# Performance work log

Hardware: AMD Instinct MI355X
Metric: run time of the kernel (lower is better)

The kernel has to match this reference:

```python
import jax, jax.numpy as jnp
import numpy as np

B, T, C = 4, 2048, 2048
N_HEAD = 16
N_KV_HEAD = 4
N_REP = N_HEAD // N_KV_HEAD  # 4
HD = C // N_HEAD             # 128
FC_MULT = 1.0
EPS = 1e-12


def l2norm(x):
    return x / (jnp.linalg.norm(x, axis=-1, keepdims=True) + EPS)


def setup_inputs() -> dict:
    key = jax.random.key(0)
    k1, k2, k3, k4 = jax.random.split(key, 4)
    s = 1.0 / np.sqrt(C)
    return {
        "x": jax.random.normal(k1, (B, T, C), dtype=jnp.float32),
        "Wq": jax.random.normal(k2, (C, C), dtype=jnp.float32) * s,
        "Wkv": jax.random.normal(k3, (C, 2 * C // N_REP), dtype=jnp.float32) * s,
        "Wproj": jax.random.normal(k4, (C, C), dtype=jnp.float32) * s,
    }


def reference(x, Wq, Wkv, Wproj):
    kv_dim = C // N_REP  # 512
    q = FC_MULT * (x @ Wq)                     # [B,T,C]
    kv = FC_MULT * (x @ Wkv)                   # [B,T,2*kv_dim]
    k, v = kv[..., :kv_dim], kv[..., kv_dim:]
    # L2 prenorm over full projection dims (before head split), as in module
    q = l2norm(q)
    k = l2norm(k)
    # split heads; GQA without materializing repeated K/V
    q = q.reshape(B, T, N_KV_HEAD, N_REP, HD)  # [B,T,G,R,H]
    k = k.reshape(B, T, N_KV_HEAD, HD)         # [B,S,G,H]
    v = v.reshape(B, T, N_KV_HEAD, HD)
    scale = 1.0 / np.sqrt(HD)
    scores = jnp.einsum('btgrh,bsgh->bgrts', q, k) * scale  # [B,G,R,T,S]
    causal = jnp.tril(jnp.ones((T, T), dtype=bool))
    scores = jnp.where(causal, scores, -jnp.inf)
    att = jax.nn.softmax(scores, axis=-1)
    y = jnp.einsum('bgrts,bsgh->btgrh', att, v)  # [B,T,G,R,H]
    y = y.reshape(B, T, C)
    return FC_MULT * (y @ Wproj)
```

## Files before the change

kernel.cpp:

```cpp
#include <hip/hip_runtime.h>
#include <hip/hip_bf16.h>
#include <math.h>

#define B_   4
#define T_   2048
#define C_   2048
#define NH_  16
#define HD_  128
#define KVD_ 1024

typedef __attribute__((ext_vector_type(4))) float f32x4;
typedef __attribute__((ext_vector_type(16))) float f32x16;
typedef __attribute__((ext_vector_type(8))) short bf16x8;
typedef __attribute__((ext_vector_type(4))) unsigned int u32x4;

__device__ __forceinline__ void async_copy16(const __hip_bfloat16* g, __hip_bfloat16* l) {
  __builtin_amdgcn_global_load_lds((const __attribute__((address_space(1))) void*)g,
                                   (__attribute__((address_space(3))) void*)l,
                                   16, 0, 0);
}

__device__ __forceinline__ float bf2f(__hip_bfloat16 h) { return __bfloat162float(h); }

__device__ __forceinline__ unsigned int pkbf(float a, float b) {
  float2 f2; f2.x = a; f2.y = b;
  __hip_bfloat162 h2 = __float22bfloat162_rn(f2);
  return *reinterpret_cast<unsigned int*>(&h2);
}

__global__ __launch_bounds__(256) void f32_to_bf16_k(const float* __restrict__ src,
                                                     __hip_bfloat16* __restrict__ dst, int n4) {
  int i = blockIdx.x * 256 + threadIdx.x;
  if (i >= n4) return;
  float4 f = ((const float4*)src)[i];
  __hip_bfloat16 o[4] = {__float2bfloat16(f.x), __float2bfloat16(f.y),
                         __float2bfloat16(f.z), __float2bfloat16(f.w)};
  *(uint2*)(dst + (size_t)i * 4) = *(uint2*)o;
}

__global__ __launch_bounds__(256) void transpose_f32_bf16_k(const float* __restrict__ W,
                                                            __hip_bfloat16* __restrict__ WT,
                                                            int K, int N) {
  __shared__ float tile[32][33];
  int bx = blockIdx.x * 32;
  int by = blockIdx.y * 32;
  int tx = threadIdx.x, ty = threadIdx.y;
  for (int i = ty; i < 32; i += 8)
    tile[i][tx] = W[(size_t)(by + i) * N + (bx + tx)];
  __syncthreads();
  for (int i = ty; i < 32; i += 8)
    WT[(size_t)(bx + i) * K + (by + tx)] = __float2bfloat16(tile[tx][i]);
}

__global__ __launch_bounds__(256) void vtrans_k(const __hip_bfloat16* __restrict__ kv,
                                                __hip_bfloat16* __restrict__ vt) {
  __shared__ __hip_bfloat16 tile[32][33];
  int bg = blockIdx.z;
  int d0 = blockIdx.y * 32;
  int t0 = blockIdx.x * 32;
  int tx = threadIdx.x, ty = threadIdx.y;
  int b = bg >> 2, g = bg & 3;
  const __hip_bfloat16* src = kv + (size_t)b * T_ * KVD_ + 512 + g * HD_;
  for (int i = ty; i < 32; i += 8)
    tile[i][tx] = src[(size_t)(t0 + i) * KVD_ + d0 + tx];
  __syncthreads();
  __hip_bfloat16* dst = vt + (size_t)bg * HD_ * T_;
  int txp = (tx & ~12) | ((tx & 4) << 1) | ((tx & 8) >> 1);
  for (int i = ty; i < 32; i += 8)
    dst[(size_t)(d0 + i) * T_ + t0 + txp] = tile[tx][i];
}

template<int PER>
__global__ __launch_bounds__(256) void rownorm_k(__hip_bfloat16* __restrict__ buf,
                                                 int stride, float extra) {
  const int tid = threadIdx.x;
  __hip_bfloat16* p = buf + (size_t)blockIdx.x * stride;
  float v[PER];
  float ss = 0.f;
  #pragma unroll
  for (int e = 0; e < PER; ++e) { v[e] = bf2f(p[tid + e * 256]); ss += v[e] * v[e]; }
  #pragma unroll
  for (int off = 32; off >= 1; off >>= 1) ss += __shfl_xor(ss, off, 64);
  __shared__ float wsum[4];
  if ((tid & 63) == 0) wsum[tid >> 6] = ss;
  __syncthreads();
  float tot = wsum[0] + wsum[1] + wsum[2] + wsum[3];
  float sc = extra / (sqrtf(tot) + 1e-12f);
  #pragma unroll
  for (int e = 0; e < PER; ++e) p[tid + e * 256] = __float2bfloat16(v[e] * sc);
}

template<typename OutT>
__global__ __launch_bounds__(512, 2) void gemm3_k(const __hip_bfloat16* __restrict__ A,
                                                  const __hip_bfloat16* __restrict__ BT,
                                                  OutT* __restrict__ Cc,
                                                  int M, int N, int K) {
  __shared__ alignas(16) __hip_bfloat16 As[3][128 * 64];
  __shared__ alignas(16) __hip_bfloat16 Bs[3][256 * 64];
  const int tid  = threadIdx.x;
  const int bm   = blockIdx.y * 128;
  const int bn   = blockIdx.x * 256;
  const int wave = tid >> 6, lane = tid & 63;
  const int wm = wave >> 2, wn = wave & 3;
  const int lm = lane & 15, quad = lane >> 4;
  const size_t Kz = (size_t)K;
  const int NT = K >> 6;

  const int srow = tid >> 3;
  const int csw  = ((tid & 7) ^ (srow & 7)) * 8;
  const __hip_bfloat16* aSrc0 = A  + (size_t)(bm + srow) * Kz + csw;
  const __hip_bfloat16* aSrc1 = A  + (size_t)(bm + 64 + srow) * Kz + csw;
  const __hip_bfloat16* bSrc0 = BT + (size_t)(bn + srow) * Kz + csw;
  const __hip_bfloat16* bSrc1 = BT + (size_t)(bn + 64 + srow) * Kz + csw;
  const __hip_bfloat16* bSrc2 = BT + (size_t)(bn + 128 + srow) * Kz + csw;
  const __hip_bfloat16* bSrc3 = BT + (size_t)(bn + 192 + srow) * Kz + csw;

  auto stageA = [&](int slot, int koff) {
    async_copy16(aSrc0 + koff, As[slot] + tid * 8);
    async_copy16(aSrc1 + koff, As[slot] + (512 + tid) * 8);
  };
  auto stageB0 = [&](int slot, int koff) {
    async_copy16(bSrc0 + koff, Bs[slot] + tid * 8);
  };
  auto stageB123 = [&](int slot, int koff) {
    async_copy16(bSrc1 + koff, Bs[slot] + (512 + tid) * 8);
    async_copy16(bSrc2 + koff, Bs[slot] + (1024 + tid) * 8);
    async_copy16(bSrc3 + koff, Bs[slot] + (1536 + tid) * 8);
  };

  const int ch0 = ((quad) ^ (lm & 7)) * 8;
  const int ch1 = ((4 + quad) ^ (lm & 7)) * 8;
  const int arow = wm * 64 + lm;
  const int brow = wn * 64 + lm;

  f32x4 acc[4][4] = {};

  stageA(0, 0); stageB0(0, 0); stageB123(0, 0);
  if (NT > 1) { stageA(1, 64); stageB0(1, 64); stageB123(1, 64); }

  int s = 0;
  for (int t = 0; t < NT; ++t) {
    const int sn = (s + 2 > 2) ? (s - 1) : (s + 2);
    const bool pre = (t + 2) < NT;
    const int koff = (t + 2) * 64;
    if (t + 1 < NT) asm volatile("s_waitcnt vmcnt(6)" ::: "memory");
    else            asm volatile("s_waitcnt vmcnt(0)" ::: "memory");
    __builtin_amdgcn_s_barrier();
    bf16x8 af[4][2], bf0[2][2];
    #pragma unroll
    for (int mf = 0; mf < 4; ++mf) {
      af[mf][0] = *(const bf16x8*)(As[s] + (arow + mf * 16) * 64 + ch0);
      af[mf][1] = *(const bf16x8*)(As[s] + (arow + mf * 16) * 64 + ch1);
    }
    #pragma unroll
    for (int nf = 0; nf < 2; ++nf) {
      bf0[nf][0] = *(const bf16x8*)(Bs[s] + (brow + nf * 16) * 64 + ch0);
      bf0[nf][1] = *(const bf16x8*)(Bs[s] + (brow + nf * 16) * 64 + ch1);
    }
    if (pre) { stageA(sn, koff); stageB0(sn, koff); }
    __builtin_amdgcn_s_barrier();
    __builtin_amdgcn_s_setprio(1);
    #pragma unroll
    for (int mf = 0; mf < 4; ++mf)
      #pragma unroll
      for (int nf = 0; nf < 2; ++nf) {
        acc[mf][nf] = __builtin_amdgcn_mfma_f32_16x16x32_bf16(af[mf][0], bf0[nf][0], acc[mf][nf], 0, 0, 0);
        acc[mf][nf] = __builtin_amdgcn_mfma_f32_16x16x32_bf16(af[mf][1], bf0[nf][1], acc[mf][nf], 0, 0, 0);
      }
    __builtin_amdgcn_s_setprio(0);
    __builtin_amdgcn_s_barrier();
    bf16x8 bf1[2][2];
    #pragma unroll
    for (int nf = 0; nf < 2; ++nf) {
      bf1[nf][0] = *(const bf16x8*)(Bs[s] + (brow + (nf + 2) * 16) * 64 + ch0);
      bf1[nf][1] = *(const bf16x8*)(Bs[s] + (brow + (nf + 2) * 16) * 64 + ch1);
    }
    if (pre) stageB123(sn, koff);
    __builtin_amdgcn_s_barrier();
    __builtin_amdgcn_s_setprio(1);
    #pragma unroll
    for (int mf = 0; mf < 4; ++mf)
      #pragma unroll
      for (int nf = 0; nf < 2; ++nf) {
        acc[mf][nf + 2] = __builtin_amdgcn_mfma_f32_16x16x32_bf16(af[mf][0], bf1[nf][0], acc[mf][nf + 2], 0, 0, 0);
        acc[mf][nf + 2] = __builtin_amdgcn_mfma_f32_16x16x32_bf16(af[mf][1], bf1[nf][1], acc[mf][nf + 2], 0, 0, 0);
      }
    __builtin_amdgcn_s_setprio(0);
    s = (s == 2) ? 0 : s + 1;
  }

  const int r0 = quad * 4;
  #pragma unroll
  for (int mf = 0; mf < 4; ++mf)
    #pragma unroll
    for (int nf = 0; nf < 4; ++nf)
      #pragma unroll
      for (int r = 0; r < 4; ++r) {
        int gr = bm + wm * 64 + mf * 16 + r0 + r;
        int gc = bn + wn * 64 + nf * 16 + lm;
        float v = acc[mf][nf][r];
        if constexpr (__is_same(OutT, float))
          Cc[(size_t)gr * N + gc] = v;
        else
          Cc[(size_t)gr * N + gc] = __float2bfloat16(v);
      }
}

__global__ __launch_bounds__(256, 2) void attn_k(const __hip_bfloat16* __restrict__ q,
                                                 const __hip_bfloat16* __restrict__ kv,
                                                 const __hip_bfloat16* __restrict__ vt,
                                                 __hip_bfloat16* __restrict__ y) {
  const int pp = blockIdx.x;
  const int h  = blockIdx.y;
  const int b  = blockIdx.z;
  const int g  = h >> 2;
  const int tid = threadIdx.x;
  const int wave = tid >> 6, lane = tid & 63;
  const int l31 = lane & 31, hi = lane >> 5;

  __shared__ alignas(16) __hip_bfloat16 Ks[2][64 * 128];
  __shared__ alignas(16) __hip_bfloat16 Vts[2][128 * 64];

  const __hip_bfloat16* kb = kv + (size_t)b * T_ * KVD_ + g * HD_;
  const __hip_bfloat16* vb = vt + (size_t)(b * 4 + g) * HD_ * T_;

  auto stage = [&](int buf, int jt) {
    const size_t j1 = (size_t)jt * 64;
    #pragma unroll
    for (int e = 0; e < 4; ++e) {
      int idx = tid + e * 256;
      int row = idx >> 4, c = idx & 15;
      async_copy16(kb + (j1 + row) * KVD_ + ((c ^ (row & 15)) * 8), Ks[buf] + idx * 8);
    }
    #pragma unroll
    for (int e = 0; e < 4; ++e) {
      int idx = tid + e * 256;
      int row = idx >> 3, c = idx & 7;
      async_copy16(vb + (size_t)row * T_ + j1 + ((c ^ (row & 7)) * 8), Vts[buf] + idx * 8);
    }
  };

  stage(0, 0);

  #pragma unroll
  for (int seg = 0; seg < 2; ++seg) {
    const int qt = seg ? pp : (15 - pp);
    const int qbase = qt * 128 + wave * 32;
    const int qmax = qbase + 31;
    const int ntiles = 2 * qt + 2;

    const __hip_bfloat16* qrow = q + ((size_t)b * T_ + qbase + l31) * C_ + h * HD_;
    bf16x8 qf[8];
    #pragma unroll
    for (int kc = 0; kc < 8; ++kc)
      qf[kc] = *(const bf16x8*)(qrow + kc * 16 + hi * 8);

    __syncthreads();

    f32x16 o_acc[4] = {};
    float l_acc = 0.f;

    for (int it = 0; it < ntiles; ++it) {
      const int cur = it & 1;
      if (it + 1 < ntiles) stage(cur ^ 1, it + 1);
      const int j0 = it * 64;
      if (j0 <= qmax) {
        f32x16 st0 = {}, st1 = {};
        __builtin_amdgcn_s_setprio(1);
        #pragma unroll
        for (int kc = 0; kc < 8; ++kc) {
          const int cs0 = (((2 * kc + hi) ^ (l31 & 15)) * 8);
          bf16x8 k0 = *(const bf16x8*)(Ks[cur] + l31 * 128 + cs0);
          bf16x8 k1 = *(const bf16x8*)(Ks[cur] + (32 + l31) * 128 + cs0);
          st0 = __builtin_amdgcn_mfma_f32_32x32x16_bf16(k0, qf[kc], st0, 0, 0, 0);
          st1 = __builtin_amdgcn_mfma_f32_32x32x16_bf16(k1, qf[kc], st1, 0, 0, 0);
        }
        __builtin_amdgcn_s_setprio(0);
        const int qd = qbase + l31 - j0;
        if (j0 + 63 <= qbase) {
          #pragma unroll
          for (int r = 0; r < 16; ++r) {
            float p0 = __expf(st0[r]);
            float p1 = __expf(st1[r]);
            st0[r] = p0; st1[r] = p1;
            l_acc += p0 + p1;
          }
        } else {
          #pragma unroll
          for (int r = 0; r < 16; ++r) {
            const int ofs = (r & 3) + 8 * (r >> 2) + 4 * hi;
            float p0 = (ofs <= qd) ? __expf(st0[r]) : 0.f;
            float p1 = (ofs + 32 <= qd) ? __expf(st1[r]) : 0.f;
            st0[r] = p0; st1[r] = p1;
            l_acc += p0 + p1;
          }
        }
        unsigned int W[8][2];
        #pragma unroll
        for (int q4 = 0; q4 < 4; ++q4) {
          W[q4][0]     = pkbf(st0[4 * q4 + 0], st0[4 * q4 + 1]);
          W[q4][1]     = pkbf(st0[4 * q4 + 2], st0[4 * q4 + 3]);
          W[4 + q4][0] = pkbf(st1[4 * q4 + 0], st1[4 * q4 + 1]);
          W[4 + q4][1] = pkbf(st1[4 * q4 + 2], st1[4 * q4 + 3]);
        }
        __builtin_amdgcn_s_setprio(1);
        #pragma unroll
        for (int kc = 0; kc < 4; ++kc) {
          u32x4 pw;
          pw[0] = W[2 * kc][0]; pw[1] = W[2 * kc][1];
          pw[2] = W[2 * kc + 1][0]; pw[3] = W[2 * kc + 1][1];
          bf16x8 pf = __builtin_bit_cast(bf16x8, pw);
          const int csv = (((2 * kc + hi) ^ (l31 & 7)) * 8);
          #pragma unroll
          for (int ct = 0; ct < 4; ++ct) {
            bf16x8 vf = *(const bf16x8*)(Vts[cur] + (ct * 32 + l31) * 64 + csv);
            o_acc[ct] = __builtin_amdgcn_mfma_f32_32x32x16_bf16(pf, vf, o_acc[ct], 0, 0, 0);
          }
        }
        __builtin_amdgcn_s_setprio(0);
      }
      __syncthreads();
    }

    if (seg == 0) stage(0, 0);

    float lsum = l_acc + __shfl_xor(l_acc, 32, 64);
    float oinv[16];
    #pragma unroll
    for (int r = 0; r < 16; ++r) {
      int row = (r & 3) + 8 * (r >> 2) + 4 * hi;
      oinv[r] = 1.0f / __shfl(lsum, row, 64);
    }
    __hip_bfloat16* yb = y + ((size_t)b * T_ + qbase) * C_ + h * HD_ + l31;
    #pragma unroll
    for (int ct = 0; ct < 4; ++ct)
      #pragma unroll
      for (int r = 0; r < 16; ++r) {
        int row = (r & 3) + 8 * (r >> 2) + 4 * hi;
        yb[(size_t)row * C_ + ct * 32] = __float2bfloat16(o_acc[ct][r] * oinv[r]);
      }
  }
}

extern "C" void kernel_launch(void* const* d_in, const int* in_sizes, int n_in,
                              void* d_out, int out_size, void* d_ws, size_t ws_size,
                              hipStream_t stream) {
  (void)in_sizes; (void)n_in; (void)out_size; (void)ws_size;
  const float* x     = (const float*)d_in[0];
  const float* Wq    = (const float*)d_in[1];
  const float* Wkv   = (const float*)d_in[2];
  const float* Wproj = (const float*)d_in[3];
  char* ws = (char*)d_ws;
  __hip_bfloat16* xb     = (__hip_bfloat16*)(ws);
  __hip_bfloat16* WqT    = (__hip_bfloat16*)(ws + 33554432);
  __hip_bfloat16* WkvT   = (__hip_bfloat16*)(ws + 41943040);
  __hip_bfloat16* WprojT = (__hip_bfloat16*)(ws + 46137344);
  __hip_bfloat16* qn     = (__hip_bfloat16*)(ws + 54525952);
  __hip_bfloat16* kvb    = (__hip_bfloat16*)(ws + 88080384);
  __hip_bfloat16* y      = xb;
  __hip_bfloat16* vt     = (__hip_bfloat16*)d_out;
  float* out             = (float*)d_out;

  f32_to_bf16_k<<<16384, 256, 0, stream>>>(x, xb, 4194304);
  transpose_f32_bf16_k<<<dim3(64, 64), dim3(32, 8), 0, stream>>>(Wq, WqT, 2048, 2048);
  transpose_f32_bf16_k<<<dim3(32, 64), dim3(32, 8), 0, stream>>>(Wkv, WkvT, 2048, 1024);
  transpose_f32_bf16_k<<<dim3(64, 64), dim3(32, 8), 0, stream>>>(Wproj, WprojT, 2048, 2048);
  gemm3_k<__hip_bfloat16><<<dim3(8, 64), 512, 0, stream>>>(xb, WqT, qn, 8192, 2048, 2048);
  gemm3_k<__hip_bfloat16><<<dim3(4, 64), 512, 0, stream>>>(xb, WkvT, kvb, 8192, 1024, 2048);
  rownorm_k<8><<<8192, 256, 0, stream>>>(qn, 2048, 0.08838834764831845f);
  rownorm_k<2><<<8192, 256, 0, stream>>>(kvb, 1024, 1.0f);
  vtrans_k<<<dim3(64, 4, 16), dim3(32, 8), 0, stream>>>(kvb, vt);
  attn_k<<<dim3(8, 16, 4), 256, 0, stream>>>(qn, kvb, vt, y);
  gemm3_k<float><<<dim3(8, 64), 512, 0, stream>>>(y, WprojT, out, 8192, 2048, 2048);
}
```

Baseline: 466.9 us.

## Split attention KV tile across two wave groups with LDS reduction

Doubles the attention block to 512 threads. Each of two wave groups processes half of every 64-key tile, so each wave does one score MFMA chain instead of two, and the partial O accumulators and row sums are combined through LDS at the end. This adds waves to hide MFMA and exp latency and cuts per-wave register pressure. In exchange it adds extra barriers, an LDS reduction of the output accumulators, and duplicate Q-fragment loads per group.

After: 478.6 us. 2.5% more time.

```diff
diff --git a/kernel.cpp b/kernel.cpp
--- a/kernel.cpp
+++ b/kernel.cpp
@@ -206,7 +206,7 @@
       }
 }
 
-__global__ __launch_bounds__(256, 2) void attn_k(const __hip_bfloat16* __restrict__ q,
+__global__ __launch_bounds__(512, 2) void attn_k(const __hip_bfloat16* __restrict__ q,
                                                  const __hip_bfloat16* __restrict__ kv,
                                                  const __hip_bfloat16* __restrict__ vt,
                                                  __hip_bfloat16* __restrict__ y) {
@@ -217,6 +217,9 @@
   const int tid = threadIdx.x;
   const int wave = tid >> 6, lane = tid & 63;
   const int l31 = lane & 31, hi = lane >> 5;
+  const int wq = wave & 3;
+  const int grp = wave >> 2;
+  const int kvofs = grp * 32;
 
   __shared__ alignas(16) __hip_bfloat16 Ks[2][64 * 128];
   __shared__ alignas(16) __hip_bfloat16 Vts[2][128 * 64];
@@ -227,14 +230,14 @@
   auto stage = [&](int buf, int jt) {
     const size_t j1 = (size_t)jt * 64;
     #pragma unroll
-    for (int e = 0; e < 4; ++e) {
-      int idx = tid + e * 256;
+    for (int e = 0; e < 2; ++e) {
+      int idx = tid + e * 512;
       int row = idx >> 4, c = idx & 15;
       async_copy16(kb + (j1 + row) * KVD_ + ((c ^ (row & 15)) * 8), Ks[buf] + idx * 8);
     }
     #pragma unroll
-    for (int e = 0; e < 4; ++e) {
-      int idx = tid + e * 256;
+    for (int e = 0; e < 2; ++e) {
+      int idx = tid + e * 512;
       int row = idx >> 3, c = idx & 7;
       async_copy16(vb + (size_t)row * T_ + j1 + ((c ^ (row & 7)) * 8), Vts[buf] + idx * 8);
     }
@@ -245,7 +248,7 @@
   #pragma unroll
   for (int seg = 0; seg < 2; ++seg) {
     const int qt = seg ? pp : (15 - pp);
-    const int qbase = qt * 128 + wave * 32;
+    const int qbase = qt * 128 + wq * 32;
     const int qmax = qbase + 31;
     const int ntiles = 2 * qt + 2;
 
@@ -263,52 +266,47 @@
     for (int it = 0; it < ntiles; ++it) {
       const int cur = it & 1;
       if (it + 1 < ntiles) stage(cur ^ 1, it + 1);
-      const int j0 = it * 64;
-      if (j0 <= qmax) {
-        f32x16 st0 = {}, st1 = {};
+      const int j0k = it * 64 + kvofs;
+      if (j0k <= qmax) {
+        f32x16 st = {};
         __builtin_amdgcn_s_setprio(1);
         #pragma unroll
         for (int kc = 0; kc < 8; ++kc) {
           const int cs0 = (((2 * kc + hi) ^ (l31 & 15)) * 8);
-          bf16x8 k0 = *(const bf16x8*)(Ks[cur] + l31 * 128 + cs0);
-          bf16x8 k1 = *(const bf16x8*)(Ks[cur] + (32 + l31) * 128 + cs0);
-          st0 = __builtin_amdgcn_mfma_f32_32x32x16_bf16(k0, qf[kc], st0, 0, 0, 0);
-          st1 = __builtin_amdgcn_mfma_f32_32x32x16_bf16(k1, qf[kc], st1, 0, 0, 0);
+          bf16x8 kf = *(const bf16x8*)(Ks[cur] + (kvofs + l31) * 128 + cs0);
+          st = __builtin_amdgcn_mfma_f32_32x32x16_bf16(kf, qf[kc], st, 0, 0, 0);
         }
         __builtin_amdgcn_s_setprio(0);
-        const int qd = qbase + l31 - j0;
-        if (j0 + 63 <= qbase) {
+        const int qd = qbase + l31 - j0k;
+        if (j0k + 31 <= qbase) {
           #pragma unroll
           for (int r = 0; r < 16; ++r) {
-            float p0 = __expf(st0[r]);
-            float p1 = __expf(st1[r]);
-            st0[r] = p0; st1[r] = p1;
-            l_acc += p0 + p1;
+            float p0 = __expf(st[r]);
+            st[r] = p0;
+            l_acc += p0;
           }
         } else {
           #pragma unroll
           for (int r = 0; r < 16; ++r) {
             const int ofs = (r & 3) + 8 * (r >> 2) + 4 * hi;
-            float p0 = (ofs <= qd) ? __expf(st0[r]) : 0.f;
-            float p1 = (ofs + 32 <= qd) ? __expf(st1[r]) : 0.f;
-            st0[r] = p0; st1[r] = p1;
-            l_acc += p0 + p1;
+            float p0 = (ofs <= qd) ? __expf(st[r]) : 0.f;
+            st[r] = p0;
+            l_acc += p0;
           }
         }
-        unsigned int W[8][2];
+        unsigned int W[4][2];
         #pragma unroll
         for (int q4 = 0; q4 < 4; ++q4) {
-          W[q4][0]     = pkbf(st0[4 * q4 + 0], st0[4 * q4 + 1]);
-          W[q4][1]     = pkbf(st0[4 * q4 + 2], st0[4 * q4 + 3]);
-          W[4 + q4][0] = pkbf(st1[4 * q4 + 0], st1[4 * q4 + 1]);
-          W[4 + q4][1] = pkbf(st1[4 * q4 + 2], st1[4 * q4 + 3]);
+          W[q4][0] = pkbf(st[4 * q4 + 0], st[4 * q4 + 1]);
+          W[q4][1] = pkbf(st[4 * q4 + 2], st[4 * q4 + 3]);
         }
         __builtin_amdgcn_s_setprio(1);
         #pragma unroll
-        for (int kc = 0; kc < 4; ++kc) {
+        for (int kci = 0; kci < 2; ++kci) {
+          const int kc = grp * 2 + kci;
           u32x4 pw;
-          pw[0] = W[2 * kc][0]; pw[1] = W[2 * kc][1];
-          pw[2] = W[2 * kc + 1][0]; pw[3] = W[2 * kc + 1][1];
+          pw[0] = W[2 * kci][0]; pw[1] = W[2 * kci][1];
+          pw[2] = W[2 * kci + 1][0]; pw[3] = W[2 * kci + 1][1];
           bf16x8 pf = __builtin_bit_cast(bf16x8, pw);
           const int csv = (((2 * kc + hi) ^ (l31 & 7)) * 8);
           #pragma unroll
@@ -325,20 +323,45 @@
     if (seg == 0) stage(0, 0);
 
     float lsum = l_acc + __shfl_xor(l_acc, 32, 64);
+    float* lcomb = (float*)&Ks[1][0];
+    float* r0 = (float*)&Ks[1][0];
+    float* r1 = (float*)&Vts[1][0];
+    if (grp == 1) lcomb[wq * 64 + lane] = lsum;
+    __syncthreads();
+    if (grp == 0) lsum += lcomb[wq * 64 + lane];
+    __syncthreads();
+
     float oinv[16];
-    #pragma unroll
-    for (int r = 0; r < 16; ++r) {
-      int row = (r & 3) + 8 * (r >> 2) + 4 * hi;
-      oinv[r] = 1.0f / __shfl(lsum, row, 64);
-    }
-    __hip_bfloat16* yb = y + ((size_t)b * T_ + qbase) * C_ + h * HD_ + l31;
-    #pragma unroll
-    for (int ct = 0; ct < 4; ++ct)
+    if (grp == 0) {
       #pragma unroll
       for (int r = 0; r < 16; ++r) {
         int row = (r & 3) + 8 * (r >> 2) + 4 * hi;
-        yb[(size_t)row * C_ + ct * 32] = __float2bfloat16(o_acc[ct][r] * oinv[r]);
-      }
+        oinv[r] = 1.0f / __shfl(lsum, row, 64);
+      }
+    }
+    __hip_bfloat16* yb = y + ((size_t)b * T_ + qbase) * C_ + h * HD_ + l31;
+    #pragma unroll
+    for (int rd = 0; rd < 2; ++rd) {
+      const int c0 = rd * 2;
+      if (grp == 1) {
+        *(f32x16*)(r0 + (wq * 64 + lane) * 16) = o_acc[c0];
+        *(f32x16*)(r1 + (wq * 64 + lane) * 16) = o_acc[c0 + 1];
+      }
+      __syncthreads();
+      if (grp == 0) {
+        f32x16 p0 = *(const f32x16*)(r0 + (wq * 64 + lane) * 16);
+        f32x16 p1 = *(const f32x16*)(r1 + (wq * 64 + lane) * 16);
+        #pragma unroll
+        for (int r = 0; r < 16; ++r) {
+          int row = (r & 3) + 8 * (r >> 2) + 4 * hi;
+          yb[(size_t)row * C_ + c0 * 32] =
+              __float2bfloat16((o_acc[c0][r] + p0[r]) * oinv[r]);
+          yb[(size_t)row * C_ + (c0 + 1) * 32] =
+              __float2bfloat16((o_acc[c0 + 1][r] + p1[r]) * oinv[r]);
+        }
+      }
+      __syncthreads();
+    }
   }
 }
 
@@ -370,6 +393,6 @@
   rownorm_k<8><<<8192, 256, 0, stream>>>(qn, 2048, 0.08838834764831845f);
   rownorm_k<2><<<8192, 256, 0, stream>>>(kvb, 1024, 1.0f);
   vtrans_k<<<dim3(64, 4, 16), dim3(32, 8), 0, stream>>>(kvb, vt);
-  attn_k<<<dim3(8, 16, 4), 256, 0, stream>>>(qn, kvb, vt, y);
+  attn_k<<<dim3(8, 16, 4), 512, 0, stream>>>(qn, kvb, vt, y);
   gemm3_k<float><<<dim3(8, 64), 512, 0, stream>>>(y, WprojT, out, 8192, 2048, 2048);
 }
```

## Enlarge GEMM block tile to 256x256 with double-buffered LDS pipeline

Applied to the files above, without the earlier changes.

The projection GEMMs now use 256x256 output tiles per 512-thread block, with each wave computing a 128x64 sub-tile (8x4 MFMA fragments), instead of 128x256 tiles. Staging changes from a three-deep to a two-deep LDS ring, with loads for the next K slice issued in two halves that are interleaved with the MFMA phases. The larger tile is meant to raise arithmetic intensity and cut global and LDS traffic per FLOP. In exchange, occupancy drops to one block per CU, there are more accumulator registers, and the grid is half as large (256 or 128 blocks), which may leave some CUs idle.

Result: slower. 516.8 us (+10.7%).

```diff
diff --git a/kernel.cpp b/kernel.cpp
--- a/kernel.cpp
+++ b/kernel.cpp
@@ -91,14 +91,14 @@
 }
 
 template<typename OutT>
-__global__ __launch_bounds__(512, 2) void gemm3_k(const __hip_bfloat16* __restrict__ A,
+__global__ __launch_bounds__(512, 1) void gemm8_k(const __hip_bfloat16* __restrict__ A,
                                                   const __hip_bfloat16* __restrict__ BT,
                                                   OutT* __restrict__ Cc,
                                                   int M, int N, int K) {
-  __shared__ alignas(16) __hip_bfloat16 As[3][128 * 64];
-  __shared__ alignas(16) __hip_bfloat16 Bs[3][256 * 64];
+  __shared__ alignas(16) __hip_bfloat16 As[2][256 * 64];
+  __shared__ alignas(16) __hip_bfloat16 Bs[2][256 * 64];
   const int tid  = threadIdx.x;
-  const int bm   = blockIdx.y * 128;
+  const int bm   = blockIdx.y * 256;
   const int bn   = blockIdx.x * 256;
   const int wave = tid >> 6, lane = tid & 63;
   const int wm = wave >> 2, wn = wave & 3;
@@ -108,95 +108,118 @@
 
   const int srow = tid >> 3;
   const int csw  = ((tid & 7) ^ (srow & 7)) * 8;
-  const __hip_bfloat16* aSrc0 = A  + (size_t)(bm + srow) * Kz + csw;
-  const __hip_bfloat16* aSrc1 = A  + (size_t)(bm + 64 + srow) * Kz + csw;
-  const __hip_bfloat16* bSrc0 = BT + (size_t)(bn + srow) * Kz + csw;
-  const __hip_bfloat16* bSrc1 = BT + (size_t)(bn + 64 + srow) * Kz + csw;
-  const __hip_bfloat16* bSrc2 = BT + (size_t)(bn + 128 + srow) * Kz + csw;
-  const __hip_bfloat16* bSrc3 = BT + (size_t)(bn + 192 + srow) * Kz + csw;
-
-  auto stageA = [&](int slot, int koff) {
-    async_copy16(aSrc0 + koff, As[slot] + tid * 8);
-    async_copy16(aSrc1 + koff, As[slot] + (512 + tid) * 8);
+  const __hip_bfloat16* aQ[4];
+  const __hip_bfloat16* bQ[4];
+  #pragma unroll
+  for (int p = 0; p < 4; ++p) {
+    aQ[p] = A  + (size_t)(bm + p * 64 + srow) * Kz + csw;
+    bQ[p] = BT + (size_t)(bn + p * 64 + srow) * Kz + csw;
+  }
+  auto stageA2 = [&](int buf, int p0, int koff) {
+    async_copy16(aQ[p0] + koff,     As[buf] + (p0) * 4096 + tid * 8);
+    async_copy16(aQ[p0 + 1] + koff, As[buf] + (p0 + 1) * 4096 + tid * 8);
   };
-  auto stageB0 = [&](int slot, int koff) {
-    async_copy16(bSrc0 + koff, Bs[slot] + tid * 8);
-  };
-  auto stageB123 = [&](int slot, int koff) {
-    async_copy16(bSrc1 + koff, Bs[slot] + (512 + tid) * 8);
-    async_copy16(bSrc2 + koff, Bs[slot] + (1024 + tid) * 8);
-    async_copy16(bSrc3 + koff, Bs[slot] + (1536 + tid) * 8);
+  auto stageB2 = [&](int buf, int p0, int koff) {
+    async_copy16(bQ[p0] + koff,     Bs[buf] + (p0) * 4096 + tid * 8);
+    async_copy16(bQ[p0 + 1] + koff, Bs[buf] + (p0 + 1) * 4096 + tid * 8);
   };
 
   const int ch0 = ((quad) ^ (lm & 7)) * 8;
   const int ch1 = ((4 + quad) ^ (lm & 7)) * 8;
-  const int arow = wm * 64 + lm;
+  const int arow = wm * 128 + lm;
   const int brow = wn * 64 + lm;
 
-  f32x4 acc[4][4] = {};
-
-  stageA(0, 0); stageB0(0, 0); stageB123(0, 0);
-  if (NT > 1) { stageA(1, 64); stageB0(1, 64); stageB123(1, 64); }
-
-  int s = 0;
+  f32x4 acc[8][4] = {};
+
+  stageA2(0, 0, 0); stageA2(0, 2, 0); stageB2(0, 0, 0); stageB2(0, 2, 0);
+
+  int cur = 0;
   for (int t = 0; t < NT; ++t) {
-    const int sn = (s + 2 > 2) ? (s - 1) : (s + 2);
-    const bool pre = (t + 2) < NT;
-    const int koff = (t + 2) * 64;
-    if (t + 1 < NT) asm volatile("s_waitcnt vmcnt(6)" ::: "memory");
-    else            asm volatile("s_waitcnt vmcnt(0)" ::: "memory");
-    __builtin_amdgcn_s_barrier();
-    bf16x8 af[4][2], bf0[2][2];
+    const int nb = cur ^ 1;
+    const bool pre = (t + 1) < NT;
+    const int koff = (t + 1) * 64;
+
+    if (pre) { stageA2(nb, 0, koff); stageB2(nb, 0, koff); }
+    if (pre) asm volatile("s_waitcnt vmcnt(4)" ::: "memory");
+    else     asm volatile("s_waitcnt vmcnt(0)" ::: "memory");
+    __builtin_amdgcn_s_barrier();
+    bf16x8 af[4][2], bfA[2][2], bfB[2][2];
     #pragma unroll
     for (int mf = 0; mf < 4; ++mf) {
-      af[mf][0] = *(const bf16x8*)(As[s] + (arow + mf * 16) * 64 + ch0);
-      af[mf][1] = *(const bf16x8*)(As[s] + (arow + mf * 16) * 64 + ch1);
+      af[mf][0] = *(const bf16x8*)(As[cur] + (arow + mf * 16) * 64 + ch0);
+      af[mf][1] = *(const bf16x8*)(As[cur] + (arow + mf * 16) * 64 + ch1);
     }
     #pragma unroll
     for (int nf = 0; nf < 2; ++nf) {
-      bf0[nf][0] = *(const bf16x8*)(Bs[s] + (brow + nf * 16) * 64 + ch0);
-      bf0[nf][1] = *(const bf16x8*)(Bs[s] + (brow + nf * 16) * 64 + ch1);
-    }
-    if (pre) { stageA(sn, koff); stageB0(sn, koff); }
-    __builtin_amdgcn_s_barrier();
+      bfA[nf][0] = *(const bf16x8*)(Bs[cur] + (brow + nf * 16) * 64 + ch0);
+      bfA[nf][1] = *(const bf16x8*)(Bs[cur] + (brow + nf * 16) * 64 + ch1);
+    }
     __builtin_amdgcn_s_setprio(1);
     #pragma unroll
     for (int mf = 0; mf < 4; ++mf)
       #pragma unroll
       for (int nf = 0; nf < 2; ++nf) {
-        acc[mf][nf] = __builtin_amdgcn_mfma_f32_16x16x32_bf16(af[mf][0], bf0[nf][0], acc[mf][nf], 0, 0, 0);
-        acc[mf][nf] = __builtin_amdgcn_mfma_f32_16x16x32_bf16(af[mf][1], bf0[nf][1], acc[mf][nf], 0, 0, 0);
+        acc[mf][nf] = __builtin_amdgcn_mfma_f32_16x16x32_bf16(af[mf][0], bfA[nf][0], acc[mf][nf], 0, 0, 0);
+        acc[mf][nf] = __builtin_amdgcn_mfma_f32_16x16x32_bf16(af[mf][1], bfA[nf][1], acc[mf][nf], 0, 0, 0);
       }
     __builtin_amdgcn_s_setprio(0);
     __builtin_amdgcn_s_barrier();
-    bf16x8 bf1[2][2];
+
+    if (pre) { stageA2(nb, 2, koff); stageB2(nb, 2, koff); }
     #pragma unroll
     for (int nf = 0; nf < 2; ++nf) {
-      bf1[nf][0] = *(const bf16x8*)(Bs[s] + (brow + (nf + 2) * 16) * 64 + ch0);
-      bf1[nf][1] = *(const bf16x8*)(Bs[s] + (brow + (nf + 2) * 16) * 64 + ch1);
-    }
-    if (pre) stageB123(sn, koff);
-    __builtin_amdgcn_s_barrier();
+      bfB[nf][0] = *(const bf16x8*)(Bs[cur] + (brow + (nf + 2) * 16) * 64 + ch0);
+      bfB[nf][1] = *(const bf16x8*)(Bs[cur] + (brow + (nf + 2) * 16) * 64 + ch1);
+    }
     __builtin_amdgcn_s_setprio(1);
     #pragma unroll
     for (int mf = 0; mf < 4; ++mf)
       #pragma unroll
       for (int nf = 0; nf < 2; ++nf) {
-        acc[mf][nf + 2] = __builtin_amdgcn_mfma_f32_16x16x32_bf16(af[mf][0], bf1[nf][0], acc[mf][nf + 2], 0, 0, 0);
-        acc[mf][nf + 2] = __builtin_amdgcn_mfma_f32_16x16x32_bf16(af[mf][1], bf1[nf][1], acc[mf][nf + 2], 0, 0, 0);
+        acc[mf][nf + 2] = __builtin_amdgcn_mfma_f32_16x16x32_bf16(af[mf][0], bfB[nf][0], acc[mf][nf + 2], 0, 0, 0);
+        acc[mf][nf + 2] = __builtin_amdgcn_mfma_f32_16x16x32_bf16(af[mf][1], bfB[nf][1], acc[mf][nf + 2], 0, 0, 0);
       }
     __builtin_amdgcn_s_setprio(0);
-    s = (s == 2) ? 0 : s + 1;
+    __builtin_amdgcn_s_barrier();
+
+    #pragma unroll
+    for (int mf = 0; mf < 4; ++mf) {
+      af[mf][0] = *(const bf16x8*)(As[cur] + (arow + (mf + 4) * 16) * 64 + ch0);
+      af[mf][1] = *(const bf16x8*)(As[cur] + (arow + (mf + 4) * 16) * 64 + ch1);
+    }
+    __builtin_amdgcn_s_setprio(1);
+    #pragma unroll
+    for (int mf = 0; mf < 4; ++mf)
+      #pragma unroll
+      for (int nf = 0; nf < 2; ++nf) {
+        acc[mf + 4][nf] = __builtin_amdgcn_mfma_f32_16x16x32_bf16(af[mf][0], bfA[nf][0], acc[mf + 4][nf], 0, 0, 0);
+        acc[mf + 4][nf] = __builtin_amdgcn_mfma_f32_16x16x32_bf16(af[mf][1], bfA[nf][1], acc[mf + 4][nf], 0, 0, 0);
+      }
+    __builtin_amdgcn_s_setprio(0);
+    __builtin_amdgcn_s_barrier();
+
+    __builtin_amdgcn_s_setprio(1);
+    #pragma unroll
+    for (int mf = 0; mf < 4; ++mf)
+      #pragma unroll
+      for (int nf = 0; nf < 2; ++nf) {
+        acc[mf + 4][nf + 2] = __builtin_amdgcn_mfma_f32_16x16x32_bf16(af[mf][0], bfB[nf][0], acc[mf + 4][nf + 2], 0, 0, 0);
+        acc[mf + 4][nf + 2] = __builtin_amdgcn_mfma_f32_16x16x32_bf16(af[mf][1], bfB[nf][1], acc[mf + 4][nf + 2], 0, 0, 0);
+      }
+    __builtin_amdgcn_s_setprio(0);
+    __builtin_amdgcn_s_barrier();
+
+    cur = nb;
   }
 
   const int r0 = quad * 4;
   #pragma unroll
-  for (int mf = 0; mf < 4; ++mf)
+  for (int mf = 0; mf < 8; ++mf)
     #pragma unroll
     for (int nf = 0; nf < 4; ++nf)
       #pragma unroll
       for (int r = 0; r < 4; ++r) {
-        int gr = bm + wm * 64 + mf * 16 + r0 + r;
+        int gr = bm + wm * 128 + mf * 16 + r0 + r;
         int gc = bn + wn * 64 + nf * 16 + lm;
         float v = acc[mf][nf][r];
         if constexpr (__is_same(OutT, float))
@@ -365,11 +388,11 @@
   transpose_f32_bf16_k<<<dim3(64, 64), dim3(32, 8), 0, stream>>>(Wq, WqT, 2048, 2048);
   transpose_f32_bf16_k<<<dim3(32, 64), dim3(32, 8), 0, stream>>>(Wkv, WkvT, 2048, 1024);
   transpose_f32_bf16_k<<<dim3(64, 64), dim3(32, 8), 0, stream>>>(Wproj, WprojT, 2048, 2048);
-  gemm3_k<__hip_bfloat16><<<dim3(8, 64), 512, 0, stream>>>(xb, WqT, qn, 8192, 2048, 2048);
-  gemm3_k<__hip_bfloat16><<<dim3(4, 64), 512, 0, stream>>>(xb, WkvT, kvb, 8192, 1024, 2048);
+  gemm8_k<__hip_bfloat16><<<dim3(8, 32), 512, 0, stream>>>(xb, WqT, qn, 8192, 2048, 2048);
+  gemm8_k<__hip_bfloat16><<<dim3(4, 32), 512, 0, stream>>>(xb, WkvT, kvb, 8192, 1024, 2048);
   rownorm_k<8><<<8192, 256, 0, stream>>>(qn, 2048, 0.08838834764831845f);
   rownorm_k<2><<<8192, 256, 0, stream>>>(kvb, 1024, 1.0f);
   vtrans_k<<<dim3(64, 4, 16), dim3(32, 8), 0, stream>>>(kvb, vt);
   attn_k<<<dim3(8, 16, 4), 256, 0, stream>>>(qn, kvb, vt, y);
-  gemm3_k<float><<<dim3(8, 64), 512, 0, stream>>>(y, WprojT, out, 8192, 2048, 2048);
-}
+  gemm8_k<float><<<dim3(8, 32), 512, 0, stream>>>(y, WprojT, out, 8192, 2048, 2048);
+}
```
